# Kernel optimization log

Hardware: AMD Instinct MI355X
Metric: run time of the kernel (lower is better)

The kernel has to match this reference:

```python
import jax, jax.numpy as jnp
import numpy as np

D = 1536          # model dim
N = 12            # num heads
HD = D // N       # head dim = 128
C = HD // 2       # rope complex channels = 64
F, H, W = 4, 32, 32
L = F * H * W     # 4096 tokens
B = 1
S1 = C - 2 * (C // 3)   # 22 channels for the frame axis
S2 = C // 3             # 21 channels each for h and w axes
EPS = 1e-6


def setup_inputs() -> dict:
    key = jax.random.key(0)
    ks = jax.random.split(key, 9)
    sc = 1.0 / np.sqrt(D)
    inp = {"x": jax.random.normal(ks[0], (B, L, D), jnp.float32)}
    for i, name in enumerate(["wq", "wk", "wv", "wo"]):
        inp[name] = jax.random.normal(ks[1 + i], (D, D), jnp.float32) * sc
    for i, name in enumerate(["bq", "bk", "bv", "bo"]):
        inp[name] = jax.random.normal(ks[5 + i], (D,), jnp.float32) * 0.01
    inp["gq"] = jnp.ones((D,), jnp.float32)
    inp["gk"] = jnp.ones((D,), jnp.float32)
    # precomputed rotary tables: angle[pos, j] = pos * theta_j (complex freqs = cos + i sin)
    pos = jnp.arange(1024, dtype=jnp.float32)
    inv = 10000.0 ** (-jnp.arange(C, dtype=jnp.float32) / C)
    ang = pos[:, None] * inv[None, :]
    inp["freqs_cos"] = jnp.cos(ang)
    inp["freqs_sin"] = jnp.sin(ang)
    inp["seq_lens"] = jnp.full((B,), L, dtype=jnp.int32)
    inp["f_size"] = F
    inp["h_size"] = H
    inp["w_size"] = W
    return inp


def _rms(y, g):
    return y * jax.lax.rsqrt(jnp.mean(y * y, axis=-1, keepdims=True) + EPS) * g


def _grid(tab, f, h, w):
    # concat per-axis frequency bands: [f,h,w, S1 | S2 | rest] -> [L, 1, C]
    a = jnp.broadcast_to(tab[:f, None, None, :S1], (f, h, w, S1))
    b = jnp.broadcast_to(tab[None, :h, None, S1:S1 + S2], (f, h, w, S2))
    c = jnp.broadcast_to(tab[None, None, :w, S1 + S2:], (f, h, w, C - S1 - S2))
    return jnp.concatenate([a, b, c], axis=-1).reshape(f * h * w, 1, C)


def reference(x, wq, bq, wk, bk, wv, bv, wo, bo, gq, gk,
              freqs_cos, freqs_sin, seq_lens, f_size, h_size, w_size):
    b, l, dim = x.shape
    n = N
    d = dim // n
    c = d // 2
    # QKV projections with QK RMSNorm (norm over full model dim, as in the module)
    q = _rms(x @ wq.T + bq, gq).reshape(b, l, n, d)
    k = _rms(x @ wk.T + bk, gk).reshape(b, l, n, d)
    v = (x @ wv.T + bv).reshape(b, l, n, d)
    # 3D rotary: complex multiply by per-position grid frequencies
    cosg = _grid(freqs_cos, f_size, h_size, w_size)  # [L,1,C]
    sing = _grid(freqs_sin, f_size, h_size, w_size)

    def rope(t):
        tr = t.reshape(b, l, n, c, 2)
        xr, xi = tr[..., 0], tr[..., 1]
        return jnp.stack([xr * cosg - xi * sing, xr * sing + xi * cosg], axis=-1).reshape(b, l, n, d)

    q = rope(q)
    k = rope(k)
    # full (non-windowed) scaled dot-product attention, all k_lens == L
    scores = jnp.einsum('blnd,bmnd->bnlm', q, k) / jnp.sqrt(jnp.float32(d))
    attn = jax.nn.softmax(scores, axis=-1)
    out = jnp.einsum('bnlm,bmnd->blnd', attn, v).reshape(b, l, dim)
    return out @ wo.T + bo
```

## Files before the change

kernel.cpp:

```cpp
#include <hip/hip_runtime.h>
#include <math.h>

#define Dm   1536
#define NHd  12
#define HDm  128
#define Ltok 4096
#define S1c  22
#define S2c  21
#define MFIX 5.0f
#define LOG2E 1.4426950408889634f

typedef __attribute__((ext_vector_type(8))) _Float16 f16x8;
typedef __attribute__((ext_vector_type(4))) float f32x4;

static __device__ __forceinline__ f32x4 MFMA16(f16x8 a, f16x8 b, f32x4 c) {
  return __builtin_amdgcn_mfma_f32_16x16x32_f16(a, b, c, 0, 0, 0);
}

static __device__ __forceinline__ unsigned int pack_f16(float a, float b) {
  union { _Float16 h[2]; unsigned int u; } x;
  x.h[0] = (_Float16)a; x.h[1] = (_Float16)b;
  return x.u;
}

static __device__ __forceinline__ void gload_lds16(const void* g, void* l) {
  __builtin_amdgcn_global_load_lds(
      (const __attribute__((address_space(1))) unsigned int*)g,
      (__attribute__((address_space(3))) unsigned int*)l, 16, 0, 0);
}

__global__ __launch_bounds__(256) void cvt_f16(
    const float* __restrict__ src, unsigned short* __restrict__ dst, int nslots)
{
  int i = blockIdx.x * 256 + threadIdx.x;
  if (i >= nslots) return;
  float4 v = *(const float4*)&src[(size_t)i * 4];
  uint2 p;
  p.x = pack_f16(v.x, v.y);
  p.y = pack_f16(v.z, v.w);
  *(uint2*)&dst[(size_t)i * 4] = p;
}

__global__ __launch_bounds__(256) void cvt_w4_f16(
    const float* __restrict__ w0, const float* __restrict__ w1,
    const float* __restrict__ w2, const float* __restrict__ w3,
    unsigned short* __restrict__ dst)
{
  const int which = blockIdx.y;
  const float* src = (which == 0) ? w0 : (which == 1) ? w1 : (which == 2) ? w2 : w3;
  unsigned short* d = dst + (size_t)which * Dm * Dm;
  int i = blockIdx.x * 256 + threadIdx.x;
  float4 v = *(const float4*)&src[(size_t)i * 4];
  uint2 p;
  p.x = pack_f16(v.x, v.y);
  p.y = pack_f16(v.z, v.w);
  *(uint2*)&d[(size_t)i * 4] = p;
}

__global__ __launch_bounds__(256) void gemm_qkv_f16(
    const unsigned short* __restrict__ Ag, const unsigned short* __restrict__ Wg,
    const float* __restrict__ bq, const float* __restrict__ bk,
    const float* __restrict__ bv,
    float* __restrict__ qb, float* __restrict__ kb,
    unsigned short* __restrict__ vT)
{
  __shared__ __align__(16) unsigned short As[128][32], Bs[128][32];
  const int tid = threadIdx.x;
  const int w = tid >> 6, lane = tid & 63;
  const int nx = lane & 15, g = lane >> 4;
  const int m0 = blockIdx.y * 128, n0 = blockIdx.x * 128;
  const int wr = w >> 1, wc = w & 1;
  const int which = (n0 >= 2 * Dm) ? 2 : ((n0 >= Dm) ? 1 : 0);
  const int n0loc = n0 - which * Dm;

  const int srow = lane >> 2, scol = (lane & 3) * 8;
  const unsigned short* gp;
  char* lbase;
  if (w < 2) {
    gp = Ag + (size_t)(m0 + w * 64 + srow) * Dm + scol;
    lbase = (char*)&As[0][0] + w * 4096;
  } else {
    gp = Wg + (size_t)(n0 + (w - 2) * 64 + srow) * Dm + scol;
    lbase = (char*)&Bs[0][0] + (w - 2) * 4096;
  }

  f32x4 acc[4][4];
#pragma unroll
  for (int i = 0; i < 4; i++)
#pragma unroll
    for (int j = 0; j < 4; j++) acc[i][j] = (f32x4){0.f, 0.f, 0.f, 0.f};

  for (int it = 0; it < Dm / 32; ++it) {
    __syncthreads();
#pragma unroll
    for (int c = 0; c < 4; ++c)
      gload_lds16(gp + (size_t)c * 16 * Dm, lbase + c * 1024);
    gp += 32;
    __syncthreads();
    f16x8 ah[4], bh[4];
#pragma unroll
    for (int i = 0; i < 4; ++i) {
      ah[i] = *(const f16x8*)&As[wr * 64 + i * 16 + nx][g * 8];
      bh[i] = *(const f16x8*)&Bs[wc * 64 + i * 16 + nx][g * 8];
    }
#pragma unroll
    for (int i = 0; i < 4; ++i)
#pragma unroll
      for (int j = 0; j < 4; ++j)
        acc[i][j] = MFMA16(ah[i], bh[j], acc[i][j]);
  }

  if (which < 2) {
    float* Cout = which ? kb : qb;
    const float* bias = which ? bk : bq;
#pragma unroll
    for (int j = 0; j < 4; ++j) {
      const int col = n0loc + wc * 64 + j * 16 + nx;
      const float bz = bias[col];
#pragma unroll
      for (int i = 0; i < 4; ++i) {
        const int row0 = m0 + wr * 64 + i * 16 + g * 4;
#pragma unroll
        for (int r = 0; r < 4; ++r)
          Cout[(size_t)(row0 + r) * Dm + col] = acc[i][j][r] + bz;
      }
    }
  } else {
#pragma unroll
    for (int j = 0; j < 4; ++j) {
      const int col = n0loc + wc * 64 + j * 16 + nx;
      const float bz = bv[col];
#pragma unroll
      for (int i = 0; i < 4; ++i) {
        const int row0 = m0 + wr * 64 + i * 16 + g * 4;
        uint2 pk;
        pk.x = pack_f16(acc[i][j][0] + bz, acc[i][j][1] + bz);
        pk.y = pack_f16(acc[i][j][2] + bz, acc[i][j][3] + bz);
        *(uint2*)&vT[(size_t)col * Ltok + row0] = pk;
      }
    }
  }
}

__global__ __launch_bounds__(256) void gemm_nt_f16(
    const unsigned short* __restrict__ Ag, const unsigned short* __restrict__ Wg,
    const float* __restrict__ bias, float* __restrict__ Cout)
{
  __shared__ __align__(16) unsigned short As[128][32], Bs[128][32];
  const int tid = threadIdx.x;
  const int w = tid >> 6, lane = tid & 63;
  const int nx = lane & 15, g = lane >> 4;
  const int m0 = blockIdx.y * 128, n0 = blockIdx.x * 128;
  const int wr = w >> 1, wc = w & 1;

  const int srow = lane >> 2, scol = (lane & 3) * 8;
  const unsigned short* gp;
  char* lbase;
  if (w < 2) {
    gp = Ag + (size_t)(m0 + w * 64 + srow) * Dm + scol;
    lbase = (char*)&As[0][0] + w * 4096;
  } else {
    gp = Wg + (size_t)(n0 + (w - 2) * 64 + srow) * Dm + scol;
    lbase = (char*)&Bs[0][0] + (w - 2) * 4096;
  }

  f32x4 acc[4][4];
#pragma unroll
  for (int i = 0; i < 4; i++)
#pragma unroll
    for (int j = 0; j < 4; j++) acc[i][j] = (f32x4){0.f, 0.f, 0.f, 0.f};

  for (int it = 0; it < Dm / 32; ++it) {
    __syncthreads();
#pragma unroll
    for (int c = 0; c < 4; ++c)
      gload_lds16(gp + (size_t)c * 16 * Dm, lbase + c * 1024);
    gp += 32;
    __syncthreads();
    f16x8 ah[4], bh[4];
#pragma unroll
    for (int i = 0; i < 4; ++i) {
      ah[i] = *(const f16x8*)&As[wr * 64 + i * 16 + nx][g * 8];
      bh[i] = *(const f16x8*)&Bs[wc * 64 + i * 16 + nx][g * 8];
    }
#pragma unroll
    for (int i = 0; i < 4; ++i)
#pragma unroll
      for (int j = 0; j < 4; ++j)
        acc[i][j] = MFMA16(ah[i], bh[j], acc[i][j]);
  }
#pragma unroll
  for (int j = 0; j < 4; ++j) {
    const int col = n0 + wc * 64 + j * 16 + nx;
    const float bz = bias[col];
#pragma unroll
    for (int i = 0; i < 4; ++i) {
      const int row0 = m0 + wr * 64 + i * 16 + g * 4;
#pragma unroll
      for (int r = 0; r < 4; ++r)
        Cout[(size_t)(row0 + r) * Dm + col] = acc[i][j][r] + bz;
    }
  }
}

__global__ __launch_bounds__(256) void rmsnorm_rope_f16(
    float* __restrict__ q, float* __restrict__ k,
    const float* __restrict__ gq, const float* __restrict__ gk,
    const float* __restrict__ fcos, const float* __restrict__ fsin)
{
  const int l = blockIdx.x;
  const int tid = threadIdx.x;
  const int d0 = tid * 6;
  float qv[6], kv[6];
  float sq = 0.f, sk = 0.f;
  const float* qp = &q[(size_t)l * Dm + d0];
  const float* kp = &k[(size_t)l * Dm + d0];
#pragma unroll
  for (int i = 0; i < 6; i++) {
    qv[i] = qp[i]; sq += qv[i] * qv[i];
    kv[i] = kp[i]; sk += kv[i] * kv[i];
  }
#pragma unroll
  for (int s = 1; s < 64; s <<= 1) {
    sq += __shfl_xor(sq, s);
    sk += __shfl_xor(sk, s);
  }
  __shared__ float redq[4], redk[4];
  if ((tid & 63) == 0) { redq[tid >> 6] = sq; redk[tid >> 6] = sk; }
  __syncthreads();
  sq = redq[0] + redq[1] + redq[2] + redq[3];
  sk = redk[0] + redk[1] + redk[2] + redk[3];
  const float rq = rsqrtf(sq * (1.f / (float)Dm) + 1e-6f);
  const float rk = rsqrtf(sk * (1.f / (float)Dm) + 1e-6f);
  const float qscale = 0.08838834764831845f * LOG2E;
  const int f = l >> 10, h = (l >> 5) & 31, w = l & 31;
  unsigned short* qo = (unsigned short*)q + (size_t)l * Dm;
  unsigned short* ko = (unsigned short*)k + (size_t)l * Dm;
#pragma unroll
  for (int i = 0; i < 3; i++) {
    const int d = d0 + 2 * i;
    const int cc = (d & (HDm - 1)) >> 1;
    const int pos = (cc < S1c) ? f : ((cc < S1c + S2c) ? h : w);
    const float co = fcos[pos * 64 + cc];
    const float si = fsin[pos * 64 + cc];
    const float xr = qv[2 * i]     * rq * gq[d];
    const float xi = qv[2 * i + 1] * rq * gq[d + 1];
    *(unsigned int*)&qo[d] =
        pack_f16((xr * co - xi * si) * qscale, (xr * si + xi * co) * qscale);
    const float yr = kv[2 * i]     * rk * gk[d];
    const float yi = kv[2 * i + 1] * rk * gk[d + 1];
    *(unsigned int*)&ko[d] = pack_f16(yr * co - yi * si, yr * si + yi * co);
  }
}

__global__ __launch_bounds__(256, 3) void attn_f16(
    const unsigned short* __restrict__ qs, const unsigned short* __restrict__ ks,
    const unsigned short* __restrict__ vT,
    float* __restrict__ Op0, float* __restrict__ Op1,
    float* __restrict__ stats)
{
  __shared__ __align__(16) unsigned short Ks[2][32][136];
  __shared__ __align__(16) unsigned short Vs[2][144][40];
  __shared__ __align__(16) unsigned short Ps[4][32][40];

  const int tid = threadIdx.x;
  const int w = tid >> 6, lane = tid & 63;
  const int nx = lane & 15, g = lane >> 4;
  const int head = blockIdx.y;
  const int half = blockIdx.z;
  const int qbase = blockIdx.x * 128 + w * 32;
  const int kvbase = half * (Ltok / 2);
  float* __restrict__ Op = half ? Op1 : Op0;

  const float NEGMFIX2 = -MFIX * LOG2E;

  for (int i = tid; i < 2 * 16 * 40; i += 256) {
    const int b = i / 640, rem = i - b * 640;
    const int r = rem / 40, cc = rem - r * 40;
    Vs[b][128 + r][cc] =
        (r == 0 && cc < 32) ? (unsigned short)0x3C00 : (unsigned short)0;
  }

  f16x8 qf[2][4];
#pragma unroll
  for (int s = 0; s < 2; s++) {
    const unsigned short* qp =
        &qs[(size_t)(qbase + s * 16 + nx) * Dm + head * HDm + g * 8];
#pragma unroll
    for (int c = 0; c < 4; c++) qf[s][c] = *(const f16x8*)(qp + c * 32);
  }

  f32x4 oacc[2][9];
#pragma unroll
  for (int s = 0; s < 2; s++)
#pragma unroll
    for (int nt = 0; nt < 9; nt++) oacc[s][nt] = (f32x4){0.f, 0.f, 0.f, 0.f};

  const int krow = tid >> 3, kchb = (tid & 7) << 4;
  const int vrow = tid >> 1, vseg = (tid & 1) << 4;

  const unsigned short* kg = &ks[(size_t)(kvbase + krow) * Dm + head * HDm + kchb];
  const unsigned short* vg = &vT[((size_t)head * HDm + vrow) * Ltok + kvbase + vseg];

  {
    uint4 ka = *(const uint4*)kg, kb4 = *(const uint4*)(kg + 8);
    uint4 va = *(const uint4*)vg, vb4 = *(const uint4*)(vg + 8);
    *(uint4*)&Ks[0][krow][kchb]     = ka;
    *(uint4*)&Ks[0][krow][kchb + 8] = kb4;
    *(uint4*)&Vs[0][vrow][vseg]     = va;
    *(uint4*)&Vs[0][vrow][vseg + 8] = vb4;
  }
  __syncthreads();

  const int NIT = Ltok / 2 / 32;
  for (int t = 0; t < NIT; t++) {
    const int cur = t & 1, nxt = cur ^ 1;
    const bool pref = (t + 1 < NIT);
    uint4 ka, kb4, va, vb4;
    if (pref) {
      kg += 32 * Dm;
      vg += 32;
      ka  = *(const uint4*)kg;  kb4 = *(const uint4*)(kg + 8);
      va  = *(const uint4*)vg;  vb4 = *(const uint4*)(vg + 8);
    }

    f32x4 sa[2][2];
#pragma unroll
    for (int s = 0; s < 2; s++)
#pragma unroll
      for (int mt = 0; mt < 2; mt++)
        sa[s][mt] = (f32x4){NEGMFIX2, NEGMFIX2, NEGMFIX2, NEGMFIX2};
#pragma unroll
    for (int c = 0; c < 4; c++) {
      f16x8 k0f = *(const f16x8*)&Ks[cur][nx][c * 32 + g * 8];
      f16x8 k1f = *(const f16x8*)&Ks[cur][16 + nx][c * 32 + g * 8];
#pragma unroll
      for (int s = 0; s < 2; s++) {
        sa[s][0] = MFMA16(k0f, qf[s][c], sa[s][0]);
        sa[s][1] = MFMA16(k1f, qf[s][c], sa[s][1]);
      }
    }

#pragma unroll
    for (int s = 0; s < 2; s++) {
      float p[8];
#pragma unroll
      for (int r = 0; r < 4; r++) {
        p[r]     = exp2f(sa[s][0][r]);
        p[4 + r] = exp2f(sa[s][1][r]);
      }
#pragma unroll
      for (int mt = 0; mt < 2; mt++) {
        unsigned int u0 = pack_f16(p[4 * mt + 0], p[4 * mt + 1]);
        unsigned int u1 = pack_f16(p[4 * mt + 2], p[4 * mt + 3]);
        *(uint2*)&Ps[w][s * 16 + nx][mt * 16 + g * 4] = make_uint2(u0, u1);
      }
    }
    __builtin_amdgcn_sched_barrier(0);

    f16x8 ph[2];
#pragma unroll
    for (int s = 0; s < 2; s++)
      ph[s] = *(const f16x8*)&Ps[w][s * 16 + nx][g * 8];
#pragma unroll
    for (int nt = 0; nt < 9; nt++) {
      f16x8 vh = *(const f16x8*)&Vs[cur][nt * 16 + nx][g * 8];
#pragma unroll
      for (int s = 0; s < 2; s++)
        oacc[s][nt] = MFMA16(ph[s], vh, oacc[s][nt]);
    }

    if (pref) {
      *(uint4*)&Ks[nxt][krow][kchb]     = ka;
      *(uint4*)&Ks[nxt][krow][kchb + 8] = kb4;
      *(uint4*)&Vs[nxt][vrow][vseg]     = va;
      *(uint4*)&Vs[nxt][vrow][vseg + 8] = vb4;
    }
    __syncthreads();
  }

#pragma unroll
  for (int s = 0; s < 2; s++) {
#pragma unroll
    for (int nt = 0; nt < 8; nt++)
#pragma unroll
      for (int r = 0; r < 4; r++)
        Op[(size_t)(qbase + s * 16 + g * 4 + r) * Dm + head * HDm + nt * 16 + nx] =
            oacc[s][nt][r];
    if (nx == 0) {
#pragma unroll
      for (int r = 0; r < 4; r++)
        stats[((size_t)half * Ltok + qbase + s * 16 + g * 4 + r) * NHd + head] =
            oacc[s][8][r];
    }
  }
}

__global__ __launch_bounds__(384) void combine_f16(
    const float* __restrict__ Op0, const float* __restrict__ Op1,
    const float* __restrict__ stats, unsigned short* __restrict__ oh)
{
  const int row = blockIdx.x;
  const int c4 = threadIdx.x * 4;
  const int head = c4 >> 7;
  const float l0 = stats[(size_t)row * NHd + head];
  const float l1 = stats[((size_t)Ltok + row) * NHd + head];
  const float rl = 1.f / (l0 + l1);
  float4 o0 = *(const float4*)&Op0[(size_t)row * Dm + c4];
  float4 o1 = *(const float4*)&Op1[(size_t)row * Dm + c4];
  uint2 p;
  p.x = pack_f16((o0.x + o1.x) * rl, (o0.y + o1.y) * rl);
  p.y = pack_f16((o0.z + o1.z) * rl, (o0.w + o1.w) * rl);
  *(uint2*)&oh[(size_t)row * Dm + c4] = p;
}

extern "C" void kernel_launch(void* const* d_in, const int* in_sizes, int n_in,
                              void* d_out, int out_size, void* d_ws, size_t ws_size,
                              hipStream_t stream)
{
  const float* x    = (const float*)d_in[0];
  const float* wq   = (const float*)d_in[1];
  const float* wk   = (const float*)d_in[2];
  const float* wv   = (const float*)d_in[3];
  const float* wo   = (const float*)d_in[4];
  const float* bq   = (const float*)d_in[5];
  const float* bk   = (const float*)d_in[6];
  const float* bv   = (const float*)d_in[7];
  const float* bo   = (const float*)d_in[8];
  const float* gq   = (const float*)d_in[9];
  const float* gk   = (const float*)d_in[10];
  const float* fcos = (const float*)d_in[11];
  const float* fsin = (const float*)d_in[12];
  float* out = (float*)d_out;

  const size_t LD = (size_t)Ltok * Dm;
  const size_t WH = (size_t)Dm * Dm;
  float* base = (float*)d_ws;
  float* qb = base;
  float* kb = base + LD;
  unsigned short* vT  = (unsigned short*)(base + 2 * LD);
  unsigned short* xh  = (unsigned short*)(base + 2 * LD + LD / 2);
  float* Op0 = base + 2 * LD + LD / 2;
  float* Op1 = Op0 + LD;
  unsigned short* wqh = (unsigned short*)(Op1 + LD);
  unsigned short* woh = wqh + 3 * WH;
  unsigned short* oh  = (unsigned short*)base;
  float* stats = (float*)(wqh + 4 * WH);

  const int xslots = (int)(LD / 4);
  const int w4     = (int)(WH / 4);
  dim3 gqkv(3 * Dm / 128, Ltok / 128);
  dim3 gout(Dm / 128, Ltok / 128);

  cvt_f16<<<(xslots + 255) / 256, 256, 0, stream>>>(x, xh, xslots);
  cvt_w4_f16<<<dim3(w4 / 256, 4), 256, 0, stream>>>(wq, wk, wv, wo, wqh);

  gemm_qkv_f16<<<gqkv, 256, 0, stream>>>(xh, wqh, bq, bk, bv, qb, kb, vT);
  rmsnorm_rope_f16<<<Ltok, 256, 0, stream>>>(qb, kb, gq, gk, fcos, fsin);
  attn_f16<<<dim3(Ltok / 128, NHd, 2), 256, 0, stream>>>(
      (const unsigned short*)qb, (const unsigned short*)kb, vT, Op0, Op1, stats);
  combine_f16<<<Ltok, 384, 0, stream>>>(Op0, Op1, stats, oh);
  gemm_nt_f16<<<gout, 256, 0, stream>>>(oh, woh, bo, out);
}
```

Baseline: 416.1 us.

## Double-buffer GEMM LDS tiles and use register ones-vector for softmax rowsum

Both GEMM kernels now use double-buffered LDS tiles. The next K-slice is issued as an async global-to-LDS load while the current slice is consumed, which removes one barrier per iteration and lets memory latency overlap with MFMA work. In the attention kernel, the row-sum column of ones is no longer stored in LDS: the ninth V tile is replaced by a register constant vector, shrinking LDS and dropping the init loop. exp2f is swapped for the hardware exp2 builtin, trading a little accuracy and denormal handling for fewer instructions.

Result: no change. 409.6 us (-1.6%).

```diff
diff --git a/kernel.cpp b/kernel.cpp
--- a/kernel.cpp
+++ b/kernel.cpp
@@ -64,7 +64,7 @@
     float* __restrict__ qb, float* __restrict__ kb,
     unsigned short* __restrict__ vT)
 {
-  __shared__ __align__(16) unsigned short As[128][32], Bs[128][32];
+  __shared__ __align__(16) unsigned short As[2][128][32], Bs[2][128][32];
   const int tid = threadIdx.x;
   const int w = tid >> 6, lane = tid & 63;
   const int nx = lane & 15, g = lane >> 4;
@@ -75,13 +75,13 @@
 
   const int srow = lane >> 2, scol = (lane & 3) * 8;
   const unsigned short* gp;
-  char* lbase;
+  char* lbase0;
   if (w < 2) {
     gp = Ag + (size_t)(m0 + w * 64 + srow) * Dm + scol;
-    lbase = (char*)&As[0][0] + w * 4096;
+    lbase0 = (char*)&As[0][0][0] + w * 4096;
   } else {
     gp = Wg + (size_t)(n0 + (w - 2) * 64 + srow) * Dm + scol;
-    lbase = (char*)&Bs[0][0] + (w - 2) * 4096;
+    lbase0 = (char*)&Bs[0][0][0] + (w - 2) * 4096;
   }
 
   f32x4 acc[4][4];
@@ -90,24 +90,34 @@
 #pragma unroll
     for (int j = 0; j < 4; j++) acc[i][j] = (f32x4){0.f, 0.f, 0.f, 0.f};
 
-  for (int it = 0; it < Dm / 32; ++it) {
-    __syncthreads();
-#pragma unroll
-    for (int c = 0; c < 4; ++c)
-      gload_lds16(gp + (size_t)c * 16 * Dm, lbase + c * 1024);
-    gp += 32;
-    __syncthreads();
+#pragma unroll
+  for (int c = 0; c < 4; ++c)
+    gload_lds16(gp + (size_t)c * 16 * Dm, lbase0 + c * 1024);
+  gp += 32;
+  __syncthreads();
+
+  const int NK = Dm / 32;
+  for (int it = 0; it < NK; ++it) {
+    const int cur = it & 1;
+    if (it + 1 < NK) {
+      char* lb = lbase0 + (cur ^ 1) * 8192;
+#pragma unroll
+      for (int c = 0; c < 4; ++c)
+        gload_lds16(gp + (size_t)c * 16 * Dm, lb + c * 1024);
+      gp += 32;
+    }
     f16x8 ah[4], bh[4];
 #pragma unroll
     for (int i = 0; i < 4; ++i) {
-      ah[i] = *(const f16x8*)&As[wr * 64 + i * 16 + nx][g * 8];
-      bh[i] = *(const f16x8*)&Bs[wc * 64 + i * 16 + nx][g * 8];
+      ah[i] = *(const f16x8*)&As[cur][wr * 64 + i * 16 + nx][g * 8];
+      bh[i] = *(const f16x8*)&Bs[cur][wc * 64 + i * 16 + nx][g * 8];
     }
 #pragma unroll
     for (int i = 0; i < 4; ++i)
 #pragma unroll
       for (int j = 0; j < 4; ++j)
         acc[i][j] = MFMA16(ah[i], bh[j], acc[i][j]);
+    __syncthreads();
   }
 
   if (which < 2) {
@@ -146,7 +156,7 @@
     const unsigned short* __restrict__ Ag, const unsigned short* __restrict__ Wg,
     const float* __restrict__ bias, float* __restrict__ Cout)
 {
-  __shared__ __align__(16) unsigned short As[128][32], Bs[128][32];
+  __shared__ __align__(16) unsigned short As[2][128][32], Bs[2][128][32];
   const int tid = threadIdx.x;
   const int w = tid >> 6, lane = tid & 63;
   const int nx = lane & 15, g = lane >> 4;
@@ -155,13 +165,13 @@
 
   const int srow = lane >> 2, scol = (lane & 3) * 8;
   const unsigned short* gp;
-  char* lbase;
+  char* lbase0;
   if (w < 2) {
     gp = Ag + (size_t)(m0 + w * 64 + srow) * Dm + scol;
-    lbase = (char*)&As[0][0] + w * 4096;
+    lbase0 = (char*)&As[0][0][0] + w * 4096;
   } else {
     gp = Wg + (size_t)(n0 + (w - 2) * 64 + srow) * Dm + scol;
-    lbase = (char*)&Bs[0][0] + (w - 2) * 4096;
+    lbase0 = (char*)&Bs[0][0][0] + (w - 2) * 4096;
   }
 
   f32x4 acc[4][4];
@@ -170,24 +180,34 @@
 #pragma unroll
     for (int j = 0; j < 4; j++) acc[i][j] = (f32x4){0.f, 0.f, 0.f, 0.f};
 
-  for (int it = 0; it < Dm / 32; ++it) {
-    __syncthreads();
-#pragma unroll
-    for (int c = 0; c < 4; ++c)
-      gload_lds16(gp + (size_t)c * 16 * Dm, lbase + c * 1024);
-    gp += 32;
-    __syncthreads();
+#pragma unroll
+  for (int c = 0; c < 4; ++c)
+    gload_lds16(gp + (size_t)c * 16 * Dm, lbase0 + c * 1024);
+  gp += 32;
+  __syncthreads();
+
+  const int NK = Dm / 32;
+  for (int it = 0; it < NK; ++it) {
+    const int cur = it & 1;
+    if (it + 1 < NK) {
+      char* lb = lbase0 + (cur ^ 1) * 8192;
+#pragma unroll
+      for (int c = 0; c < 4; ++c)
+        gload_lds16(gp + (size_t)c * 16 * Dm, lb + c * 1024);
+      gp += 32;
+    }
     f16x8 ah[4], bh[4];
 #pragma unroll
     for (int i = 0; i < 4; ++i) {
-      ah[i] = *(const f16x8*)&As[wr * 64 + i * 16 + nx][g * 8];
-      bh[i] = *(const f16x8*)&Bs[wc * 64 + i * 16 + nx][g * 8];
+      ah[i] = *(const f16x8*)&As[cur][wr * 64 + i * 16 + nx][g * 8];
+      bh[i] = *(const f16x8*)&Bs[cur][wc * 64 + i * 16 + nx][g * 8];
     }
 #pragma unroll
     for (int i = 0; i < 4; ++i)
 #pragma unroll
       for (int j = 0; j < 4; ++j)
         acc[i][j] = MFMA16(ah[i], bh[j], acc[i][j]);
+    __syncthreads();
   }
 #pragma unroll
   for (int j = 0; j < 4; ++j) {
@@ -260,7 +280,7 @@
     float* __restrict__ stats)
 {
   __shared__ __align__(16) unsigned short Ks[2][32][136];
-  __shared__ __align__(16) unsigned short Vs[2][144][40];
+  __shared__ __align__(16) unsigned short Vs[2][128][40];
   __shared__ __align__(16) unsigned short Ps[4][32][40];
 
   const int tid = threadIdx.x;
@@ -274,12 +294,9 @@
 
   const float NEGMFIX2 = -MFIX * LOG2E;
 
-  for (int i = tid; i < 2 * 16 * 40; i += 256) {
-    const int b = i / 640, rem = i - b * 640;
-    const int r = rem / 40, cc = rem - r * 40;
-    Vs[b][128 + r][cc] =
-        (r == 0 && cc < 32) ? (unsigned short)0x3C00 : (unsigned short)0;
-  }
+  f16x8 vones;
+#pragma unroll
+  for (int i = 0; i < 8; i++) vones[i] = (_Float16)1.0f;
 
   f16x8 qf[2][4];
 #pragma unroll
@@ -346,8 +363,8 @@
       float p[8];
 #pragma unroll
       for (int r = 0; r < 4; r++) {
-        p[r]     = exp2f(sa[s][0][r]);
-        p[4 + r] = exp2f(sa[s][1][r]);
+        p[r]     = __builtin_amdgcn_exp2f(sa[s][0][r]);
+        p[4 + r] = __builtin_amdgcn_exp2f(sa[s][1][r]);
       }
 #pragma unroll
       for (int mt = 0; mt < 2; mt++) {
@@ -363,12 +380,15 @@
     for (int s = 0; s < 2; s++)
       ph[s] = *(const f16x8*)&Ps[w][s * 16 + nx][g * 8];
 #pragma unroll
-    for (int nt = 0; nt < 9; nt++) {
+    for (int nt = 0; nt < 8; nt++) {
       f16x8 vh = *(const f16x8*)&Vs[cur][nt * 16 + nx][g * 8];
 #pragma unroll
       for (int s = 0; s < 2; s++)
         oacc[s][nt] = MFMA16(ph[s], vh, oacc[s][nt]);
     }
+#pragma unroll
+    for (int s = 0; s < 2; s++)
+      oacc[s][8] = MFMA16(ph[s], vones, oacc[s][8]);
 
     if (pref) {
       *(uint4*)&Ks[nxt][krow][kchb]     = ka;
```
